# Optimization experiments

Measured on AMD Instinct MI355X. Metric: run time of the kernel, lower is better.

Reference implementation:

```python
import jax, jax.numpy as jnp
import numpy as np

OUT = (4, 4, 4)       # output_size
SCALE = 1.0           # spatial_scale


def _axis_masks(start, length, n_bins, dim):
    """PyTorch AdaptiveMaxPool bin membership along one axis.

    bin i covers global indices [start + floor(i*L/O), start + ceil((i+1)*L/O)).
    Returns bool mask of shape [N, n_bins, dim].
    """
    i = jnp.arange(n_bins)
    bs = start[:, None] + (i[None, :] * length[:, None]) // n_bins
    be = start[:, None] - ((-(i[None, :] + 1) * length[:, None]) // n_bins)  # ceil div
    p = jnp.arange(dim)
    return (p[None, None, :] >= bs[:, :, None]) & (p[None, None, :] < be[:, :, None])


def _roi_pool_3d(x, rois):
    feat = x[0]                     # [C, X, Y, Z]
    C, X, Y, Z = feat.shape
    # rois: [1, N, 7] = (batch_idx, x0, y0, z0, x1, y1, z1); scale + round as in torch code
    r = jnp.round(rois[0, :, 1:].astype(jnp.float32) * SCALE).astype(jnp.int32)  # [N, 6]
    starts = r[:, :3]               # [N, 3]
    lens = r[:, 3:] + 1 - starts    # inclusive ends -> lengths, >= 1
    O1, O2, O3 = OUT
    mx = _axis_masks(starts[:, 0], lens[:, 0], O1, X)   # [N, O1, X]
    my = _axis_masks(starts[:, 1], lens[:, 1], O2, Y)   # [N, O2, Y]
    mz = _axis_masks(starts[:, 2], lens[:, 2], O3, Z)   # [N, O3, Z]
    neg = jnp.finfo(feat.dtype).min
    # separable max-reductions: z, then y, then x (loops are over the tiny fixed bin counts)
    t = jnp.stack([jnp.max(jnp.where(mz[:, k][:, None, None, None, :], feat[None], neg), axis=-1)
                   for k in range(O3)], axis=-1)                      # [N, C, X, Y, O3]
    t = jnp.stack([jnp.max(jnp.where(my[:, j][:, None, None, :, None], t, neg), axis=3)
                   for j in range(O2)], axis=3)                       # [N, C, X, O2, O3]
    t = jnp.stack([jnp.max(jnp.where(mx[:, i][:, None, :, None, None], t, neg), axis=2)
                   for i in range(O1)], axis=2)                       # [N, C, O1, O2, O3]
    return t


def setup_inputs() -> dict:
    key = jax.random.key(0)
    C, D, N = 64, 48, 16
    x = jax.random.normal(key, (1, C, D, D, D), dtype=jnp.float32)
    rng = np.random.default_rng(0)
    lens = rng.integers(8, 25, size=(N, 3))                       # roi extents in [8, 24]
    starts = np.array([rng.integers(0, D - L + 1) for L in lens.reshape(-1)]).reshape(N, 3)
    ends = starts + lens - 1                                      # inclusive ends, < D
    rois = np.concatenate([np.zeros((N, 1), np.int32),
                           starts.astype(np.int32),
                           ends.astype(np.int32)], axis=1)        # [N, 7]
    return {"input": x, "rois": jnp.asarray(rois[None], dtype=jnp.int32)}


def reference(input, rois):
    return _roi_pool_3d(input, rois)   # [N, C, 4, 4, 4]
```

## Files before the change

kernel.cpp:

```cpp
#include <hip/hip_runtime.h>
#include <float.h>

#define NC 64
#define DIM 48
#define NROI 16
#define D2 (DIM * DIM)

__global__ __launch_bounds__(256) void roipool3d_kernel(
    const float* __restrict__ feat,
    const int*   __restrict__ rois,
    float*       __restrict__ out)
{
    int t = threadIdx.x;
    int lane = t & 63;
    int w = (blockIdx.x << 2) | (t >> 6);
    int j = w & 3;
    int i = (w >> 2) & 3;
    int c = (w >> 4) & (NC - 1);
    int n = w >> 10;

    const int* r = rois + n * 7;
    int sx = r[1], sy = r[2], sz = r[3];
    int lx = r[4] + 1 - sx;
    int ly = r[5] + 1 - sy;
    int lz = r[6] + 1 - sz;

    int bx0 = (i * lx) >> 2, bx1 = ((i + 1) * lx + 3) >> 2;
    int by0 = (j * ly) >> 2, by1 = ((j + 1) * ly + 3) >> 2;
    int nx = bx1 - bx0, ny = by1 - by0;
    int nrows = nx * ny;

    int rp = lane >> 5;
    int zt = lane & 31;
    bool zok = (zt < lz);

    const float* base = feat + (size_t)c * (D2 * DIM)
                      + (sx + bx0) * D2 + (sy + by0) * DIM + sz + zt;

    int x = 0, y = rp, rr = rp;
    float m = -FLT_MAX;
    int rounds = (nrows + 1) >> 1;
    int batches = (rounds + 3) >> 2;
    for (int b = 0; b < batches; ++b) {
        float v0 = -FLT_MAX, v1 = -FLT_MAX, v2 = -FLT_MAX, v3 = -FLT_MAX;
        if (zok && rr < nrows) v0 = base[x * D2 + y * DIM];
        y += 2; if (y >= ny) { y -= ny; ++x; } rr += 2;
        if (zok && rr < nrows) v1 = base[x * D2 + y * DIM];
        y += 2; if (y >= ny) { y -= ny; ++x; } rr += 2;
        if (zok && rr < nrows) v2 = base[x * D2 + y * DIM];
        y += 2; if (y >= ny) { y -= ny; ++x; } rr += 2;
        if (zok && rr < nrows) v3 = base[x * D2 + y * DIM];
        y += 2; if (y >= ny) { y -= ny; ++x; } rr += 2;
        m = fmaxf(m, fmaxf(fmaxf(v0, v1), fmaxf(v2, v3)));
    }

    m = fmaxf(m, __shfl_xor(m, 32));

    int k = lane & 3;
    int zb0 = (k * lz) >> 2;
    int zb1 = ((k + 1) * lz + 3) >> 2;
    float mk = -FLT_MAX;
    #pragma unroll
    for (int s = 0; s < 7; ++s) {
        int idx = zb0 + s;
        float v = __shfl(m, idx);
        if (idx < zb1) mk = fmaxf(mk, v);
    }

    if (lane < 4)
        out[(((n << 6) | c) << 6) | (i << 4) | (j << 2) | k] = mk;
}

extern "C" void kernel_launch(void* const* d_in, const int* in_sizes, int n_in,
                              void* d_out, int out_size, void* d_ws, size_t ws_size,
                              hipStream_t stream) {
    const float* feat = (const float*)d_in[0];
    const int*   rois = (const int*)d_in[1];
    float*       out  = (float*)d_out;

    roipool3d_kernel<<<dim3(NROI * NC * 4), dim3(256), 0, stream>>>(feat, rois, out);
}
```

Measured before the change: 76.11 us.

## Split z-row across 16-lane groups with fully unrolled 4-row-parallel loads

Each wavefront now handles four (x,y) rows at a time, with 16 lanes covering z in two halves, instead of two rows with 32 lanes. The row loop is fully unrolled to 13 independent load slots, so all loads can be issued before any reduction. The goal is fewer idle lanes when the ROI z-extent is small and more memory-level parallelism. In exchange it uses more registers, needs extra shuffle reductions across the 16-lane groups, and relies on a hardcoded 13-iteration bound on the row count.

```diff
diff --git a/kernel.cpp b/kernel.cpp
--- a/kernel.cpp
+++ b/kernel.cpp
@@ -30,31 +30,45 @@
     int nx = bx1 - bx0, ny = by1 - by0;
     int nrows = nx * ny;
 
-    int rp = lane >> 5;
-    int zt = lane & 31;
-    bool zok = (zt < lz);
+    int rp = lane >> 4;
+    int zt = lane & 15;
+    bool zokl = zt < lz;
+    bool zokh = (zt + 16) < lz;
+    bool hz = lz > 16;
 
     const float* base = feat + (size_t)c * (D2 * DIM)
                       + (sx + bx0) * D2 + (sy + by0) * DIM + sz + zt;
 
     int x = 0, y = rp, rr = rp;
-    float m = -FLT_MAX;
-    int rounds = (nrows + 1) >> 1;
-    int batches = (rounds + 3) >> 2;
-    for (int b = 0; b < batches; ++b) {
-        float v0 = -FLT_MAX, v1 = -FLT_MAX, v2 = -FLT_MAX, v3 = -FLT_MAX;
-        if (zok && rr < nrows) v0 = base[x * D2 + y * DIM];
-        y += 2; if (y >= ny) { y -= ny; ++x; } rr += 2;
-        if (zok && rr < nrows) v1 = base[x * D2 + y * DIM];
-        y += 2; if (y >= ny) { y -= ny; ++x; } rr += 2;
-        if (zok && rr < nrows) v2 = base[x * D2 + y * DIM];
-        y += 2; if (y >= ny) { y -= ny; ++x; } rr += 2;
-        if (zok && rr < nrows) v3 = base[x * D2 + y * DIM];
-        y += 2; if (y >= ny) { y -= ny; ++x; } rr += 2;
-        m = fmaxf(m, fmaxf(fmaxf(v0, v1), fmaxf(v2, v3)));
+    if (y >= ny) { y -= ny; ++x; }
+
+    float va[13], vb[13];
+    #pragma unroll
+    for (int q = 0; q < 13; ++q) { va[q] = -FLT_MAX; vb[q] = -FLT_MAX; }
+
+    #pragma unroll
+    for (int q = 0; q < 13; ++q) {
+        if (4 * q >= nrows) break;
+        bool act = rr < nrows;
+        const float* p = base + x * D2 + y * DIM;
+        if (act & zokl) va[q] = p[0];
+        if (hz) { if (act & zokh) vb[q] = p[16]; }
+        y += 4;
+        if (y >= ny) { y -= ny; ++x; }
+        if (y >= ny) { y -= ny; ++x; }
+        rr += 4;
     }
 
-    m = fmaxf(m, __shfl_xor(m, 32));
+    float mlo = -FLT_MAX, mhi = -FLT_MAX;
+    #pragma unroll
+    for (int q = 0; q < 13; ++q) { mlo = fmaxf(mlo, va[q]); mhi = fmaxf(mhi, vb[q]); }
+
+    mlo = fmaxf(mlo, __shfl_xor(mlo, 16));
+    mlo = fmaxf(mlo, __shfl_xor(mlo, 32));
+    if (hz) {
+        mhi = fmaxf(mhi, __shfl_xor(mhi, 16));
+        mhi = fmaxf(mhi, __shfl_xor(mhi, 32));
+    }
 
     int k = lane & 3;
     int zb0 = (k * lz) >> 2;
@@ -63,7 +77,11 @@
     #pragma unroll
     for (int s = 0; s < 7; ++s) {
         int idx = zb0 + s;
-        float v = __shfl(m, idx);
+        float v = __shfl(mlo, idx & 15);
+        if (hz) {
+            float vh = __shfl(mhi, idx & 15);
+            if (idx >= 16) v = vh;
+        }
         if (idx < zb1) mk = fmaxf(mk, v);
     }
 
```

New measurement: 78.23 us. +2.8%, slower.
